# Performance work log

Measured on AMD Instinct MI355X. Metric: run time of the kernel, lower is better.

The kernel has to match this reference:

```python
import jax, jax.numpy as jnp
import numpy as np

NUM_NODES = 500000
NUM_RELATIONS = 500
HIDDEN = 128
R_DIM = 64
BATCH = 65536
EPS = 1e-12


def setup_inputs() -> dict:
    key = jax.random.key(0)
    k1, k2, k3, k4, k5, k6 = jax.random.split(key, 6)
    return {
        "src": jax.random.randint(k1, (BATCH,), 0, NUM_NODES, dtype=jnp.int32),
        "rel": jax.random.randint(k2, (BATCH,), 0, NUM_RELATIONS, dtype=jnp.int32),
        "dst": jax.random.randint(k3, (BATCH,), 0, NUM_NODES, dtype=jnp.int32),
        "entity_embedding": jax.random.normal(k4, (NUM_NODES, HIDDEN), dtype=jnp.float32),
        "relation_embedding": jax.random.normal(k5, (NUM_RELATIONS, R_DIM), dtype=jnp.float32),
        "projection_matrix": jax.random.normal(k6, (NUM_RELATIONS, HIDDEN, R_DIM), dtype=jnp.float32),
    }


def _l2_normalize(x):
    # F.normalize(p=2): x / max(||x||, eps)
    n = jnp.sqrt(jnp.sum(x * x, axis=-1, keepdims=True))
    return x / jnp.maximum(n, EPS)


def reference(src, rel, dst, entity_embedding, relation_embedding, projection_matrix):
    src_emb = entity_embedding[src]            # [B, H]
    dst_emb = entity_embedding[dst]            # [B, H]
    rel_emb = relation_embedding[rel]          # [B, R]
    proj = projection_matrix[rel]              # [B, H, R] per-relation gather
    src_proj = jnp.einsum("bh,bhr->br", src_emb, proj)
    dst_proj = jnp.einsum("bh,bhr->br", dst_emb, proj)
    src_proj = _l2_normalize(src_proj)
    dst_proj = _l2_normalize(dst_proj)
    diff = src_proj + rel_emb - dst_proj
    score = jnp.sqrt(jnp.sum(diff * diff, axis=-1))  # [B]
    return score
```

## Files before the change

kernel.cpp:

```cpp
#include <hip/hip_runtime.h>
#include <math.h>

#define BATCH   65536
#define NREL    500
#define HIDDEN  128
#define RDIM    64
#define EPS     1e-12f
#define SPLIT   2
#define SLOT    512
#define STHREADS 1024
#define SBLK    (BATCH / STHREADS)

#define WS_CUR_OFF  (NREL * SLOT * sizeof(int4))

typedef __attribute__((ext_vector_type(8))) short short8;
typedef __attribute__((ext_vector_type(4))) float f32x4;

__device__ __forceinline__ unsigned short f2bf(float x) {
    unsigned u = __float_as_uint(x);
    u += 0x7fffu + ((u >> 16) & 1u);
    return (unsigned short)(u >> 16);
}

__global__ __launch_bounds__(STHREADS) void sort_k(
        const int* __restrict__ rel,
        const int* __restrict__ src,
        const int* __restrict__ dst,
        unsigned*  __restrict__ cursor,
        int4*      __restrict__ sRec) {
    __shared__ unsigned lh[NREL];
    __shared__ unsigned lbase[NREL];
    __shared__ unsigned lcnt[NREL];
    const int tid = threadIdx.x;
    for (int i = tid; i < NREL; i += STHREADS) { lh[i] = 0u; lcnt[i] = 0u; }
    __syncthreads();
    const int item = blockIdx.x * STHREADS + tid;
    const int r = rel[item];
    atomicAdd(&lh[r], 1u);
    __syncthreads();
    for (int i = tid; i < NREL; i += STHREADS) {
        unsigned c = lh[i];
        if (c) lbase[i] = atomicAdd(&cursor[i], c);
    }
    __syncthreads();
    unsigned p = (unsigned)r * SLOT + lbase[r] + atomicAdd(&lcnt[r], 1u);
    sRec[p] = make_int4(item, src[item], dst[item], 0);
}

__global__ __launch_bounds__(256, 4) void proc_k(
        const float*    __restrict__ ent,
        const float*    __restrict__ relemb,
        const float*    __restrict__ proj,
        const unsigned* __restrict__ cursor,
        const int4*     __restrict__ sRec,
        float*          __restrict__ out) {
    __shared__ __align__(16) short Pt[RDIM][136];
    __shared__ __align__(16) short Ab[64][136];
    __shared__ float Rlds[RDIM];

    const int tid  = threadIdx.x;
    const int w    = tid >> 6;
    const int lane = tid & 63;
    const int rblk = blockIdx.x / SPLIT;
    const int part = blockIdx.x % SPLIT;

    const unsigned start = (unsigned)rblk * SLOT;
    const unsigned cnt   = cursor[rblk];
    const unsigned end   = start + cnt;
    if (cnt == 0) return;

    const int r_      = tid >> 2;
    const int qq      = tid & 3;
    const int sitm    = r_ >> 1;
    const int halfsel = r_ & 1;

    const int nst = (int)((cnt + 31u) >> 5);

    float4 pf[8];
    if (part < nst) {
        unsigned p = start + ((unsigned)part << 5) + (unsigned)sitm;
        if (p >= end) p = end - 1;
        int4 rec = sRec[p];
        int n = halfsel ? rec.z : rec.y;
        const float4* eg = (const float4*)(ent + (size_t)n * HIDDEN + qq * 32);
        #pragma unroll
        for (int j = 0; j < 8; j++) pf[j] = eg[j];
    }

    const float4* Pg4 = (const float4*)(proj + (size_t)rblk * (HIDDEN * RDIM));
    for (int f = tid; f < (HIDDEN * RDIM) / 4; f += 256) {
        float4 v = Pg4[f];
        int h  = f >> 4;
        int r0 = (f & 15) << 2;
        Pt[r0 + 0][h] = (short)f2bf(v.x);
        Pt[r0 + 1][h] = (short)f2bf(v.y);
        Pt[r0 + 2][h] = (short)f2bf(v.z);
        Pt[r0 + 3][h] = (short)f2bf(v.w);
    }
    if (tid < RDIM) Rlds[tid] = relemb[rblk * RDIM + tid];

    const int c    = lane & 15;
    const int g    = lane >> 4;
    const int q8   = g * 8;
    const int arow = (w << 4) + c;

    for (int t = part; t < nst; t += SPLIT) {
        const unsigned base = start + ((unsigned)t << 5);

        {
            unsigned buf[16];
            #pragma unroll
            for (int j = 0; j < 8; j++) {
                buf[2 * j]     = ((unsigned)f2bf(pf[j].y) << 16) | f2bf(pf[j].x);
                buf[2 * j + 1] = ((unsigned)f2bf(pf[j].w) << 16) | f2bf(pf[j].z);
            }
            uint4* dstp = (uint4*)&Ab[r_][qq * 32];
            #pragma unroll
            for (int s = 0; s < 4; s++) dstp[s] = ((uint4*)buf)[s];
        }
        __syncthreads();

        if (t + SPLIT < nst) {
            unsigned p = start + ((unsigned)(t + SPLIT) << 5) + (unsigned)sitm;
            if (p >= end) p = end - 1;
            int4 rec = sRec[p];
            int n = halfsel ? rec.z : rec.y;
            const float4* eg = (const float4*)(ent + (size_t)n * HIDDEN + qq * 32);
            #pragma unroll
            for (int j = 0; j < 8; j++) pf[j] = eg[j];
        }

        f32x4 acc[4];
        #pragma unroll
        for (int nt = 0; nt < 4; nt++) acc[nt] = (f32x4){0.f, 0.f, 0.f, 0.f};

        #pragma unroll
        for (int kk = 0; kk < 4; kk++) {
            short8 af = *(const short8*)&Ab[arow][kk * 32 + q8];
            #pragma unroll
            for (int nt = 0; nt < 4; nt++) {
                short8 bf = *(const short8*)&Pt[nt * 16 + c][kk * 32 + q8];
                acc[nt] = __builtin_amdgcn_mfma_f32_16x16x32_bf16(af, bf, acc[nt], 0, 0, 0);
            }
        }

        float ssq[4];
        #pragma unroll
        for (int j = 0; j < 4; j++) {
            ssq[j] = acc[0][j] * acc[0][j] + acc[1][j] * acc[1][j]
                   + acc[2][j] * acc[2][j] + acc[3][j] * acc[3][j];
        }
        #pragma unroll
        for (int m = 1; m < 16; m <<= 1) {
            #pragma unroll
            for (int j = 0; j < 4; j++) ssq[j] += __shfl_xor(ssq[j], m, 64);
        }
        float inv[4];
        #pragma unroll
        for (int j = 0; j < 4; j++) inv[j] = 1.0f / fmaxf(sqrtf(ssq[j]), EPS);

        float sa = 0.f, sb = 0.f;
        #pragma unroll
        for (int nt = 0; nt < 4; nt++) {
            float rv = Rlds[nt * 16 + c];
            float da = acc[nt][0] * inv[0] + rv - acc[nt][1] * inv[1];
            float db = acc[nt][2] * inv[2] + rv - acc[nt][3] * inv[3];
            sa = fmaf(da, da, sa);
            sb = fmaf(db, db, sb);
        }
        #pragma unroll
        for (int m = 1; m < 16; m <<= 1) {
            sa += __shfl_xor(sa, m, 64);
            sb += __shfl_xor(sb, m, 64);
        }
        if (c == 0) {
            unsigned pa = base + (unsigned)((w << 3) + (g << 1));
            if (pa < end)     out[sRec[pa].x]     = sqrtf(sa);
            if (pa + 1 < end) out[sRec[pa + 1].x] = sqrtf(sb);
        }
        __syncthreads();
    }
}

extern "C" void kernel_launch(void* const* d_in, const int* in_sizes, int n_in,
                              void* d_out, int out_size, void* d_ws, size_t ws_size,
                              hipStream_t stream) {
    (void)in_sizes; (void)n_in; (void)out_size; (void)ws_size;
    const int*   src    = (const int*)d_in[0];
    const int*   rel    = (const int*)d_in[1];
    const int*   dst    = (const int*)d_in[2];
    const float* ent    = (const float*)d_in[3];
    const float* relemb = (const float*)d_in[4];
    const float* proj   = (const float*)d_in[5];
    float*       out    = (float*)d_out;

    int4*     sRec   = (int4*)d_ws;
    unsigned* cursor = (unsigned*)((char*)d_ws + WS_CUR_OFF);

    hipMemsetAsync(cursor, 0, NREL * sizeof(unsigned), stream);
    sort_k<<<SBLK, STHREADS, 0, stream>>>(rel, src, dst, cursor, sRec);
    proc_k<<<NREL * SPLIT, 256, 0, stream>>>(ent, relemb, proj, cursor, sRec, out);
}
```

Baseline: 330.5 us.

## Use direct global atomics in sort and reorder proc block-to-relation mapping

The bucketing kernel drops its shared-memory histogram and three barriers and instead does one global atomicAdd per item on the per-relation cursor, using smaller 256-thread blocks. The processing grid is remapped so part-0 blocks for all relations come first and part-1 blocks follow at an offset of 504, with padding blocks exiting early. The intent is to cut barrier and LDS overhead in the sort and to spread each relation's two blocks apart in dispatch order. The trade-off is more contention on global atomics, about 131 updates per cursor, and a few idle blocks.

```diff
diff --git a/kernel.cpp b/kernel.cpp
--- a/kernel.cpp
+++ b/kernel.cpp
@@ -7,9 +7,8 @@
 #define RDIM    64
 #define EPS     1e-12f
 #define SPLIT   2
+#define PART1_BASE 504
 #define SLOT    512
-#define STHREADS 1024
-#define SBLK    (BATCH / STHREADS)
 
 #define WS_CUR_OFF  (NREL * SLOT * sizeof(int4))
 
@@ -22,29 +21,18 @@
     return (unsigned short)(u >> 16);
 }
 
-__global__ __launch_bounds__(STHREADS) void sort_k(
+__global__ __launch_bounds__(256) void sort_k(
         const int* __restrict__ rel,
         const int* __restrict__ src,
         const int* __restrict__ dst,
         unsigned*  __restrict__ cursor,
         int4*      __restrict__ sRec) {
-    __shared__ unsigned lh[NREL];
-    __shared__ unsigned lbase[NREL];
-    __shared__ unsigned lcnt[NREL];
-    const int tid = threadIdx.x;
-    for (int i = tid; i < NREL; i += STHREADS) { lh[i] = 0u; lcnt[i] = 0u; }
-    __syncthreads();
-    const int item = blockIdx.x * STHREADS + tid;
+    const int item = blockIdx.x * 256 + threadIdx.x;
     const int r = rel[item];
-    atomicAdd(&lh[r], 1u);
-    __syncthreads();
-    for (int i = tid; i < NREL; i += STHREADS) {
-        unsigned c = lh[i];
-        if (c) lbase[i] = atomicAdd(&cursor[i], c);
-    }
-    __syncthreads();
-    unsigned p = (unsigned)r * SLOT + lbase[r] + atomicAdd(&lcnt[r], 1u);
-    sRec[p] = make_int4(item, src[item], dst[item], 0);
+    const int s = src[item];
+    const int d = dst[item];
+    unsigned p = atomicAdd(&cursor[r], 1u);
+    sRec[(unsigned)r * SLOT + p] = make_int4(item, s, d, 0);
 }
 
 __global__ __launch_bounds__(256, 4) void proc_k(
@@ -61,8 +49,9 @@
     const int tid  = threadIdx.x;
     const int w    = tid >> 6;
     const int lane = tid & 63;
-    const int rblk = blockIdx.x / SPLIT;
-    const int part = blockIdx.x % SPLIT;
+    const int part = (blockIdx.x >= PART1_BASE) ? 1 : 0;
+    const int rblk = blockIdx.x - part * PART1_BASE;
+    if (rblk >= NREL) return;
 
     const unsigned start = (unsigned)rblk * SLOT;
     const unsigned cnt   = cursor[rblk];
@@ -198,6 +187,6 @@
     unsigned* cursor = (unsigned*)((char*)d_ws + WS_CUR_OFF);
 
     hipMemsetAsync(cursor, 0, NREL * sizeof(unsigned), stream);
-    sort_k<<<SBLK, STHREADS, 0, stream>>>(rel, src, dst, cursor, sRec);
-    proc_k<<<NREL * SPLIT, 256, 0, stream>>>(ent, relemb, proj, cursor, sRec, out);
+    sort_k<<<BATCH / 256, 256, 0, stream>>>(rel, src, dst, cursor, sRec);
+    proc_k<<<PART1_BASE + NREL, 256, 0, stream>>>(ent, relemb, proj, cursor, sRec, out);
 }
```

New measurement: 349.4 us. 5.7% more time.
